# Kernel tuning notes

Hardware: AMD Instinct MI355X
Metric: run time of the kernel (lower is better)

Reference implementation:

```python
import jax, jax.numpy as jnp
import numpy as np

B, N, D, DH = 2, 512, 64, 64


def _lin_params(key, din, dout):
    kw, kb = jax.random.split(key)
    bound = 1.0 / np.sqrt(din)
    W = jax.random.uniform(kw, (din, dout), jnp.float32, -bound, bound)
    b = jax.random.uniform(kb, (dout,), jnp.float32, -bound, bound)
    return W, b


def setup_inputs() -> dict:
    key = jax.random.key(0)
    ks = jax.random.split(key, 11)
    inp = {
        "x": jax.random.normal(ks[0], (B, N, D), jnp.float32),
        "e": jax.random.normal(ks[1], (B, N, N, D), jnp.float32),
    }
    # node-to-node self-attention: Linear(d, d_head)
    inp["Wq1"], inp["bq1"] = _lin_params(ks[2], D, DH)
    inp["Wk1"], inp["bk1"] = _lin_params(ks[3], D, DH)
    inp["Wv1"], inp["bv1"] = _lin_params(ks[4], D, DH)
    # node-to-edge cross-attention
    inp["Wqe"], inp["bqe"] = _lin_params(ks[5], D, DH)   # Q_edge: Linear(d, d_head) on e
    inp["Wkn"], inp["bkn"] = _lin_params(ks[6], DH, DH)  # K_node: Linear(d_head, d_head)
    inp["Wvn"], inp["bvn"] = _lin_params(ks[7], DH, DH)  # V_node
    # edge-to-node cross-attention (all Linear(d_head, d_head))
    inp["Wqn"], inp["bqn"] = _lin_params(ks[8], DH, DH)
    inp["Wke"], inp["bke"] = _lin_params(ks[9], DH, DH)
    inp["Wve"], inp["bve"] = _lin_params(ks[10], DH, DH)
    return inp


def _forward(x, e, Wq1, bq1, Wk1, bk1, Wv1, bv1,
             Wqe, bqe, Wkn, bkn, Wvn, bvn,
             Wqn, bqn, Wke, bke, Wve, bve):
    sqrt_d = jnp.sqrt(jnp.asarray(DH, x.dtype))
    lin = lambda z, W, b: z @ W + b

    # --- self-attention node-to-node: x (B,N,d) -> x_hat (B,N,d_head) ---
    Q = lin(x, Wq1, bq1)
    K = lin(x, Wk1, bk1)
    V = lin(x, Wv1, bv1)
    A = jax.nn.softmax(jnp.einsum('bnd,bmd->bnm', Q, K) / sqrt_d, axis=-1)
    x_hat = jnp.einsum('bnm,bmd->bnd', A, V)

    # --- cross-attention node-to-edge: update e (B,N,N,d) -> e_new (B,N,N,d_head) ---
    Qe = lin(e, Wqe, bqe)                 # (B,N,N,dh)
    Kn = lin(x_hat, Wkn, bkn)             # (B,N,dh)
    Vn = lin(x_hat, Wvn, bvn)
    Si = jnp.einsum('bijd,bjd->bij', Qe, Kn) / sqrt_d  # K_i[b,i,j] = Kn[b,j]
    Sj = jnp.einsum('bijd,bid->bij', Qe, Kn) / sqrt_d  # K_j[b,i,j] = Kn[b,i]
    # Att_i/(Att_i+Att_j) = sigmoid(Si - Sj)
    Ai = jax.nn.sigmoid(Si - Sj)
    Aj = 1.0 - Ai
    e_new = Ai[..., None] * Vn[:, None, :, :] + Aj[..., None] * Vn[:, :, None, :]

    # --- cross-attention edge-to-node: x_new (B,N,d_head) ---
    Qn = lin(x_hat, Wqn, bqn)             # (B,N,dh)
    Ke = lin(e_new, Wke, bke)             # (B,N,N,dh)
    Ve = lin(e_new, Wve, bve)
    S = jnp.einsum('bid,bijd->bij', Qn, Ke) / sqrt_d
    A2 = jax.nn.softmax(S, axis=2)
    x_new = jnp.einsum('bij,bijd->bid', A2, Ve)
    return x_new, e_new


def reference(x, e, Wq1, bq1, Wk1, bk1, Wv1, bv1,
              Wqe, bqe, Wkn, bkn, Wvn, bvn,
              Wqn, bqn, Wke, bke, Wve, bve):
    return _forward(x, e, Wq1, bq1, Wk1, bk1, Wv1, bv1,
                    Wqe, bqe, Wkn, bkn, Wvn, bvn,
                    Wqn, bqn, Wke, bke, Wve, bve)
```

## Files before the change

kernel.cpp:

```cpp
#include <hip/hip_runtime.h>
#include <math.h>

#define NN 512
#define RR 1024

typedef float f4 __attribute__((ext_vector_type(4)));

__global__ __launch_bounds__(256) void prep_kernel(
    const float* __restrict__ x,
    const float* __restrict__ Wq1, const float* __restrict__ bq1,
    const float* __restrict__ Wk1, const float* __restrict__ bk1,
    const float* __restrict__ Wv1, const float* __restrict__ bv1,
    const float* __restrict__ Wkn, const float* __restrict__ bkn,
    const float* __restrict__ Wvn, const float* __restrict__ bvn,
    const float* __restrict__ Wqe, const float* __restrict__ bqe,
    const float* __restrict__ Wke, const float* __restrict__ Wve,
    float* __restrict__ Q, float* __restrict__ K, float* __restrict__ V,
    float* __restrict__ M_P, float* __restrict__ c_P,
    float* __restrict__ M_ke, float* __restrict__ c_ke,
    float* __restrict__ M_ve, float* __restrict__ c_ve,
    float* __restrict__ vq0, float* __restrict__ s0p)
{
    __shared__ float sh[14528];
    const int t = threadIdx.x;

    if (blockIdx.x < 3) {
        const int m = blockIdx.x;
        float* As = sh;
        float* Bs = sh + 4160;
        float* va = sh + 8320;
        float* vb = sh + 8384;
        const float* A  = (m == 0) ? Wkn : Wvn;
        const float* aV = (m == 0) ? bkn : bvn;
        const float* B  = (m == 0) ? Wqe : (m == 1 ? Wke : Wve);
#pragma unroll
        for (int p = 0; p < 16; ++p) {
            const int idx = p * 256 + t;
            const int r = idx >> 6, cc = idx & 63;
            As[r * 65 + cc] = A[idx];
            if (m == 0) Bs[r * 65 + cc] = B[idx];
            else        Bs[cc * 65 + r] = B[idx];
        }
        if (t < 64) { va[t] = aV[t]; vb[t] = bqe[t]; }
        __syncthreads();

        const int b = t & 63, g = t >> 6;
        float acc[16];
#pragma unroll
        for (int aa = 0; aa < 16; ++aa) acc[aa] = 0.f;
        for (int k = 0; k < 64; ++k) {
            const float bv = Bs[b * 65 + k];
#pragma unroll
            for (int aa = 0; aa < 16; ++aa)
                acc[aa] = fmaf(As[(g * 16 + aa) * 65 + k], bv, acc[aa]);
        }
        float* M = (m == 0) ? M_P : (m == 1 ? M_ke : M_ve);
#pragma unroll
        for (int aa = 0; aa < 16; ++aa)
            M[(g * 16 + aa) * 64 + b] = acc[aa];

        if (t < 64) {
            float cb = 0.f;
            for (int k = 0; k < 64; ++k) cb = fmaf(va[k], Bs[t * 65 + k], cb);
            float* C = (m == 0) ? c_P : (m == 1 ? c_ke : c_ve);
            C[t] = cb;
            if (m == 0) {
                float q = 0.f;
                for (int k = 0; k < 64; ++k) q = fmaf(As[t * 65 + k], vb[k], q);
                vq0[t] = q * 0.125f;
            }
        }
        if (m == 0 && t == 0) {
            float s = 0.f;
            for (int k = 0; k < 64; ++k) s += vb[k] * va[k];
            *s0p = s * 0.125f;
        }
    } else {
        const int rb = (blockIdx.x - 3) * 32;
        float* Ws0 = sh;
        float* Ws1 = sh + 4096;
        float* Ws2 = sh + 8192;
        float* xs  = sh + 12288;
        float* bs0 = sh + 14336;
        float* bs1 = sh + 14400;
        float* bs2 = sh + 14464;
#pragma unroll
        for (int p = 0; p < 4; ++p) {
            const int idx = p * 256 + t;
            ((f4*)Ws0)[idx] = ((const f4*)Wq1)[idx];
            ((f4*)Ws1)[idx] = ((const f4*)Wk1)[idx];
            ((f4*)Ws2)[idx] = ((const f4*)Wv1)[idx];
        }
        ((f4*)xs)[t]       = ((const f4*)(x + rb * 64))[t];
        ((f4*)xs)[t + 256] = ((const f4*)(x + rb * 64))[t + 256];
        if (t < 64) { bs0[t] = bq1[t]; bs1[t] = bk1[t]; bs2[t] = bv1[t]; }
        __syncthreads();

        const int d = t & 63, g = t >> 6;
        float a0[8], a1[8], a2[8];
#pragma unroll
        for (int r = 0; r < 8; ++r) { a0[r] = bs0[d]; a1[r] = bs1[d]; a2[r] = bs2[d]; }
        for (int k4 = 0; k4 < 16; ++k4) {
            float w0[4], w1[4], w2[4];
#pragma unroll
            for (int kk = 0; kk < 4; ++kk) {
                w0[kk] = Ws0[(k4 * 4 + kk) * 64 + d];
                w1[kk] = Ws1[(k4 * 4 + kk) * 64 + d];
                w2[kk] = Ws2[(k4 * 4 + kk) * 64 + d];
            }
#pragma unroll
            for (int r = 0; r < 8; ++r) {
                const f4 xv = ((const f4*)xs)[(g * 8 + r) * 16 + k4];
                a0[r] = fmaf(xv.x, w0[0], fmaf(xv.y, w0[1], fmaf(xv.z, w0[2], fmaf(xv.w, w0[3], a0[r]))));
                a1[r] = fmaf(xv.x, w1[0], fmaf(xv.y, w1[1], fmaf(xv.z, w1[2], fmaf(xv.w, w1[3], a1[r]))));
                a2[r] = fmaf(xv.x, w2[0], fmaf(xv.y, w2[1], fmaf(xv.z, w2[2], fmaf(xv.w, w2[3], a2[r]))));
            }
        }
#pragma unroll
        for (int r = 0; r < 8; ++r) {
            Q[(rb + g * 8 + r) * 64 + d] = a0[r];
            K[(rb + g * 8 + r) * 64 + d] = a1[r];
            V[(rb + g * 8 + r) * 64 + d] = a2[r];
        }
    }
}

__global__ __launch_bounds__(256) void selfattn4_kernel(
    const float* __restrict__ Q, const float* __restrict__ K,
    const float* __restrict__ V, float* __restrict__ xhat)
{
    const int rb = blockIdx.x * 4;
    const int b  = rb >> 9;
    const int t  = threadIdx.x;
    const int w  = t >> 6, l = t & 63;

    __shared__ float qs[4 * 64];
    __shared__ float p[4 * 512];

    qs[t] = Q[rb * 64 + t];
    __syncthreads();

#pragma unroll
    for (int half = 0; half < 2; ++half) {
        const int j = half * 256 + t;
        const f4* kr = (const f4*)(K + (size_t)(b * NN + j) * 64);
        float s0 = 0.f, s1 = 0.f, s2 = 0.f, s3 = 0.f;
#pragma unroll
        for (int u = 0; u < 16; ++u) {
            const f4 kv = kr[u];
            const f4 qa = ((const f4*)qs)[u];
            const f4 qb = ((const f4*)(qs + 64))[u];
            const f4 qc = ((const f4*)(qs + 128))[u];
            const f4 qd = ((const f4*)(qs + 192))[u];
            s0 += kv.x * qa.x + kv.y * qa.y + kv.z * qa.z + kv.w * qa.w;
            s1 += kv.x * qb.x + kv.y * qb.y + kv.z * qb.z + kv.w * qb.w;
            s2 += kv.x * qc.x + kv.y * qc.y + kv.z * qc.z + kv.w * qc.w;
            s3 += kv.x * qd.x + kv.y * qd.y + kv.z * qd.z + kv.w * qd.w;
        }
        p[0 * 512 + j] = s0 * 0.125f;
        p[1 * 512 + j] = s1 * 0.125f;
        p[2 * 512 + j] = s2 * 0.125f;
        p[3 * 512 + j] = s3 * 0.125f;
    }
    __syncthreads();

    float* prw = p + w * 512;
    float v[8];
#pragma unroll
    for (int z = 0; z < 8; ++z) v[z] = prw[l + z * 64];
    float mx = v[0];
#pragma unroll
    for (int z = 1; z < 8; ++z) mx = fmaxf(mx, v[z]);
#pragma unroll
    for (int o = 1; o < 64; o <<= 1) mx = fmaxf(mx, __shfl_xor(mx, o));
    float se = 0.f;
#pragma unroll
    for (int z = 0; z < 8; ++z) { v[z] = expf(v[z] - mx); se += v[z]; prw[l + z * 64] = v[z]; }
#pragma unroll
    for (int o = 1; o < 64; o <<= 1) se += __shfl_xor(se, o);
    const float inv = 1.f / se;
    __syncthreads();

    const float* Vb = V + (size_t)b * NN * 64;
    float a0 = 0.f, a1 = 0.f, a2 = 0.f, a3 = 0.f;
    const f4* pw4 = (const f4*)prw;
    for (int j4 = 0; j4 < 128; ++j4) {
        const f4 pv = pw4[j4];
        const int j = j4 * 4;
        a0 = fmaf(pv.x, Vb[(j + 0) * 64 + l], a0);
        a1 = fmaf(pv.y, Vb[(j + 1) * 64 + l], a1);
        a2 = fmaf(pv.z, Vb[(j + 2) * 64 + l], a2);
        a3 = fmaf(pv.w, Vb[(j + 3) * 64 + l], a3);
    }
    xhat[(size_t)(rb + w) * 64 + l] = ((a0 + a1) + (a2 + a3)) * inv;
}

__global__ __launch_bounds__(256) void affine5_kernel(
    const float* __restrict__ xhat,
    const float* __restrict__ Wqn, const float* __restrict__ bqn,
    const float* __restrict__ Wvn, const float* __restrict__ bvn,
    const float* __restrict__ M_P, const float* __restrict__ c_P,
    const float* __restrict__ M_ke, const float* __restrict__ c_ke,
    const float* __restrict__ M_ve, const float* __restrict__ c_ve,
    const float* __restrict__ vq0, const float* __restrict__ s0p,
    float* __restrict__ Qn, float* __restrict__ Vn, float* __restrict__ P,
    float* __restrict__ VnWke, float* __restrict__ VnWve, float* __restrict__ q0)
{
    const int t = threadIdx.x;
    const int rb = blockIdx.x * 32;
    const int m = blockIdx.y;
    const float* W; const float* c; float* o;
    if (m == 0)      { W = Wqn;  c = bqn;  o = Qn; }
    else if (m == 1) { W = Wvn;  c = bvn;  o = Vn; }
    else if (m == 2) { W = M_P;  c = c_P;  o = P; }
    else if (m == 3) { W = M_ke; c = c_ke; o = VnWke; }
    else             { W = M_ve; c = c_ve; o = VnWve; }
    __shared__ float Ws[4096], xs[2048], cs[64], vq0s[64];
#pragma unroll
    for (int p = 0; p < 4; ++p) ((f4*)Ws)[p * 256 + t] = ((const f4*)W)[p * 256 + t];
    ((f4*)xs)[t]       = ((const f4*)(xhat + rb * 64))[t];
    ((f4*)xs)[t + 256] = ((const f4*)(xhat + rb * 64))[t + 256];
    if (t < 64) { cs[t] = c[t]; if (m == 0) vq0s[t] = vq0[t]; }
    __syncthreads();

    const int d = t & 63, g = t >> 6;
    float acc[8];
#pragma unroll
    for (int r = 0; r < 8; ++r) acc[r] = cs[d];
    for (int k4 = 0; k4 < 16; ++k4) {
        float w[4];
#pragma unroll
        for (int kk = 0; kk < 4; ++kk) w[kk] = Ws[(k4 * 4 + kk) * 64 + d];
#pragma unroll
        for (int r = 0; r < 8; ++r) {
            const f4 xv = ((const f4*)xs)[(g * 8 + r) * 16 + k4];
            acc[r] = fmaf(xv.x, w[0], fmaf(xv.y, w[1], fmaf(xv.z, w[2], fmaf(xv.w, w[3], acc[r]))));
        }
    }
#pragma unroll
    for (int r = 0; r < 8; ++r) o[(rb + g * 8 + r) * 64 + d] = acc[r];

    if (m == 0) {
        const int row = t >> 3, seg = t & 7;
        float part = 0.f;
#pragma unroll
        for (int kk = 0; kk < 8; ++kk)
            part = fmaf(xs[row * 64 + seg * 8 + kk], vq0s[seg * 8 + kk], part);
        part += __shfl_xor(part, 1);
        part += __shfl_xor(part, 2);
        part += __shfl_xor(part, 4);
        if (seg == 0) q0[rb + row] = part + s0p[0];
    }
}

__global__ __launch_bounds__(256, 4) void edge_kernel(
    const float* __restrict__ e, const float* __restrict__ P,
    const float* __restrict__ q0, const float* __restrict__ Vn,
    const float* __restrict__ Qn, const float* __restrict__ VnWke,
    const float* __restrict__ VnWve,
    float* __restrict__ e_new,
    float* __restrict__ Epart, float* __restrict__ Gpart, float* __restrict__ Wpart)
{
    const int blk = blockIdx.x;
    const int bi = blk >> 3;
    const int jc = blk & 7;
    const int b  = bi >> 9;
    const int t  = threadIdx.x;
    const int r  = t >> 4;
    const int k  = t & 15;

    const f4* erow  = (const f4*)(e     + (size_t)bi * NN * 64);
    f4*       enrow = (f4*)      (e_new + (size_t)bi * NN * 64);
    const f4* Prow  = (const f4*)P     + (size_t)b * NN * 16;
    const f4* Vrow  = (const f4*)Vn    + (size_t)b * NN * 16;
    const f4* Krow  = (const f4*)VnWke + (size_t)b * NN * 16;
    const f4* Wvrow = (const f4*)VnWve + (size_t)b * NN * 16;
    const float* q0b = q0 + b * NN;

    const int j0 = jc * 64 + r;
    const int j1 = j0 + 16, j2 = j0 + 32, j3 = j0 + 48;

    const f4 ev0 = erow[j0 * 16 + k];
    const f4 ev1 = erow[j1 * 16 + k];
    const f4 ev2 = erow[j2 * 16 + k];
    const f4 ev3 = erow[j3 * 16 + k];

    const float q0i = q0[bi];
    const f4 pi4 = ((const f4*)P)[bi * 16 + k];
    const f4 vi4 = ((const f4*)Vn)[bi * 16 + k];
    const f4 qn4 = ((const f4*)Qn)[bi * 16 + k];
    const f4 wi4 = ((const f4*)VnWke)[bi * 16 + k];
    float uii = qn4.x * wi4.x + qn4.y * wi4.y + qn4.z * wi4.z + qn4.w * wi4.w;
    uii += __shfl_xor(uii, 1);
    uii += __shfl_xor(uii, 2);
    uii += __shfl_xor(uii, 4);
    uii += __shfl_xor(uii, 8);
    uii *= 0.125f;

    float Eacc = 0.f, Gacc = 0.f;
    f4 Wacc = {0.f, 0.f, 0.f, 0.f};

#define EDGE_ITER(EV, J)                                                        \
    {                                                                           \
        const f4 pj = Prow[(J) * 16 + k];                                       \
        const f4 wj = Krow[(J) * 16 + k];                                       \
        const f4 vj = Vrow[(J) * 16 + k];                                       \
        const f4 wv = Wvrow[(J) * 16 + k];                                      \
        const float qj = q0b[(J)];                                              \
        float s = EV.x * (pj.x - pi4.x) + EV.y * (pj.y - pi4.y)                 \
                + EV.z * (pj.z - pi4.z) + EV.w * (pj.w - pi4.w);                \
        float uu = qn4.x * wj.x + qn4.y * wj.y + qn4.z * wj.z + qn4.w * wj.w;   \
        s  += __shfl_xor(s, 1);  uu += __shfl_xor(uu, 1);                       \
        s  += __shfl_xor(s, 2);  uu += __shfl_xor(uu, 2);                       \
        s  += __shfl_xor(s, 4);  uu += __shfl_xor(uu, 4);                       \
        s  += __shfl_xor(s, 8);  uu += __shfl_xor(uu, 8);                       \
        const float ai = 1.f / (1.f + expf(-(s * 0.125f + qj - q0i)));          \
        f4 en;                                                                  \
        en.x = fmaf(ai, vj.x - vi4.x, vi4.x);                                   \
        en.y = fmaf(ai, vj.y - vi4.y, vi4.y);                                   \
        en.z = fmaf(ai, vj.z - vi4.z, vi4.z);                                   \
        en.w = fmaf(ai, vj.w - vi4.w, vi4.w);                                   \
        __builtin_nontemporal_store(en, enrow + (J) * 16 + k);                  \
        const float ex  = expf(ai * (uu * 0.125f - uii));                       \
        const float aex = ai * ex;                                              \
        Eacc += ex;                                                             \
        Gacc += aex;                                                            \
        Wacc.x = fmaf(aex, wv.x, Wacc.x);                                       \
        Wacc.y = fmaf(aex, wv.y, Wacc.y);                                       \
        Wacc.z = fmaf(aex, wv.z, Wacc.z);                                       \
        Wacc.w = fmaf(aex, wv.w, Wacc.w);                                       \
    }

    EDGE_ITER(ev0, j0)
    EDGE_ITER(ev1, j1)
    EDGE_ITER(ev2, j2)
    EDGE_ITER(ev3, j3)
#undef EDGE_ITER

    Eacc += __shfl_xor(Eacc, 16);  Eacc += __shfl_xor(Eacc, 32);
    Gacc += __shfl_xor(Gacc, 16);  Gacc += __shfl_xor(Gacc, 32);
    Wacc.x += __shfl_xor(Wacc.x, 16);  Wacc.x += __shfl_xor(Wacc.x, 32);
    Wacc.y += __shfl_xor(Wacc.y, 16);  Wacc.y += __shfl_xor(Wacc.y, 32);
    Wacc.z += __shfl_xor(Wacc.z, 16);  Wacc.z += __shfl_xor(Wacc.z, 32);
    Wacc.w += __shfl_xor(Wacc.w, 16);  Wacc.w += __shfl_xor(Wacc.w, 32);

    __shared__ float Wred[4][65];
    __shared__ float EG[8];
    const int l = t & 63, w = t >> 6;
    if (l < 16) {
        Wred[w][l * 4 + 0] = Wacc.x;
        Wred[w][l * 4 + 1] = Wacc.y;
        Wred[w][l * 4 + 2] = Wacc.z;
        Wred[w][l * 4 + 3] = Wacc.w;
        if (l == 0) { EG[w] = Eacc; EG[4 + w] = Gacc; }
    }
    __syncthreads();
    if (t < 64) {
        const float Wsum = Wred[0][t] + Wred[1][t] + Wred[2][t] + Wred[3][t];
        Wpart[((size_t)jc * RR + bi) * 64 + t] = Wsum;
        if (t == 0) {
            Epart[jc * RR + bi] = EG[0] + EG[1] + EG[2] + EG[3];
            Gpart[jc * RR + bi] = EG[4] + EG[5] + EG[6] + EG[7];
        }
    }
}

__global__ __launch_bounds__(256) void final4_kernel(
    const float* __restrict__ Epart, const float* __restrict__ Gpart,
    const float* __restrict__ Wpart, const float* __restrict__ VnWve,
    const float* __restrict__ bve, float* __restrict__ x_new)
{
    const int bi = blockIdx.x * 4 + (threadIdx.x >> 6);
    const int t = threadIdx.x & 63;
    float Wsum = 0.f;
#pragma unroll
    for (int jc = 0; jc < 8; ++jc)
        Wsum += Wpart[((size_t)jc * RR + bi) * 64 + t];
    float E = 0.f, G = 0.f;
#pragma unroll
    for (int jc = 0; jc < 8; ++jc) {
        E += Epart[jc * RR + bi];
        G += Gpart[jc * RR + bi];
    }
    const float inv = 1.f / E;
    x_new[(size_t)bi * 64 + t] = bve[t] + VnWve[(size_t)bi * 64 + t] * (1.f - G * inv)
                               + Wsum * inv;
}

extern "C" void kernel_launch(void* const* d_in, const int* in_sizes, int n_in,
                              void* d_out, int out_size, void* d_ws, size_t ws_size,
                              hipStream_t stream) {
    const float* x   = (const float*)d_in[0];
    const float* e   = (const float*)d_in[1];
    const float* Wq1 = (const float*)d_in[2];  const float* bq1 = (const float*)d_in[3];
    const float* Wk1 = (const float*)d_in[4];  const float* bk1 = (const float*)d_in[5];
    const float* Wv1 = (const float*)d_in[6];  const float* bv1 = (const float*)d_in[7];
    const float* Wqe = (const float*)d_in[8];  const float* bqe = (const float*)d_in[9];
    const float* Wkn = (const float*)d_in[10]; const float* bkn = (const float*)d_in[11];
    const float* Wvn = (const float*)d_in[12]; const float* bvn = (const float*)d_in[13];
    const float* Wqn = (const float*)d_in[14]; const float* bqn = (const float*)d_in[15];
    const float* Wke = (const float*)d_in[16];
    const float* Wve = (const float*)d_in[18]; const float* bve = (const float*)d_in[19];

    float* out = (float*)d_out;
    float* x_new = out;
    float* e_new = out + 2 * NN * 64;

    float* ws = (float*)d_ws;
    float* Q     = ws;
    float* K     = Q + RR * 64;
    float* V     = K + RR * 64;
    float* xhat  = V + RR * 64;
    float* Qn    = xhat + RR * 64;
    float* Vn    = Qn + RR * 64;
    float* P     = Vn + RR * 64;
    float* VnWke = P + RR * 64;
    float* VnWve = VnWke + RR * 64;
    float* q0    = VnWve + RR * 64;
    float* M_P   = q0 + RR;
    float* M_ke  = M_P + 4096;
    float* M_ve  = M_ke + 4096;
    float* c_P   = M_ve + 4096;
    float* c_ke  = c_P + 64;
    float* c_ve  = c_ke + 64;
    float* vq0   = c_ve + 64;
    float* s0    = vq0 + 64;
    float* Epart = s0 + 64;
    float* Gpart = Epart + 8 * RR;
    float* Wpart = Gpart + 8 * RR;

    prep_kernel<<<35, 256, 0, stream>>>(x, Wq1, bq1, Wk1, bk1, Wv1, bv1,
                                        Wkn, bkn, Wvn, bvn, Wqe, bqe, Wke, Wve,
                                        Q, K, V,
                                        M_P, c_P, M_ke, c_ke, M_ve, c_ve, vq0, s0);
    selfattn4_kernel<<<RR / 4, 256, 0, stream>>>(Q, K, V, xhat);
    affine5_kernel<<<dim3(32, 5), 256, 0, stream>>>(xhat, Wqn, bqn, Wvn, bvn,
                                                    M_P, c_P, M_ke, c_ke, M_ve, c_ve,
                                                    vq0, s0,
                                                    Qn, Vn, P, VnWke, VnWve, q0);
    edge_kernel<<<RR * 8, 256, 0, stream>>>(e, P, q0, Vn, Qn, VnWke, VnWve,
                                            e_new, Epart, Gpart, Wpart);
    final4_kernel<<<RR / 4, 256, 0, stream>>>(Epart, Gpart, Wpart, VnWve, bve, x_new);
}
```

Before: 82.62 us.

## Process four rows per edge block to reuse per-j loads

Each edge_kernel block now handles four consecutive i rows for one j chunk instead of one, so the per-j loads of P, Vn, VnWke, VnWve and q0 are shared across four rows, and the grid shrinks fourfold. The j loop runs four iterations, each loading four e vectors. This cuts redundant gather traffic and block count but raises register pressure and lowers the number of e loads in flight per thread before compute, which may hurt latency hiding in a bandwidth-bound kernel.

```diff
diff --git a/kernel.cpp b/kernel.cpp
--- a/kernel.cpp
+++ b/kernel.cpp
@@ -262,105 +262,125 @@
     float* __restrict__ Epart, float* __restrict__ Gpart, float* __restrict__ Wpart)
 {
     const int blk = blockIdx.x;
-    const int bi = blk >> 3;
-    const int jc = blk & 7;
-    const int b  = bi >> 9;
-    const int t  = threadIdx.x;
-    const int r  = t >> 4;
-    const int k  = t & 15;
-
-    const f4* erow  = (const f4*)(e     + (size_t)bi * NN * 64);
-    f4*       enrow = (f4*)      (e_new + (size_t)bi * NN * 64);
+    const int bi0 = (blk >> 3) * 4;
+    const int jc  = blk & 7;
+    const int b   = bi0 >> 9;
+    const int t = threadIdx.x;
+    const int r = t >> 4, k = t & 15;
+    const int w = t >> 6, l = t & 63;
+
     const f4* Prow  = (const f4*)P     + (size_t)b * NN * 16;
     const f4* Vrow  = (const f4*)Vn    + (size_t)b * NN * 16;
     const f4* Krow  = (const f4*)VnWke + (size_t)b * NN * 16;
     const f4* Wvrow = (const f4*)VnWve + (size_t)b * NN * 16;
     const float* q0b = q0 + b * NN;
 
-    const int j0 = jc * 64 + r;
-    const int j1 = j0 + 16, j2 = j0 + 32, j3 = j0 + 48;
-
-    const f4 ev0 = erow[j0 * 16 + k];
-    const f4 ev1 = erow[j1 * 16 + k];
-    const f4 ev2 = erow[j2 * 16 + k];
-    const f4 ev3 = erow[j3 * 16 + k];
-
-    const float q0i = q0[bi];
-    const f4 pi4 = ((const f4*)P)[bi * 16 + k];
-    const f4 vi4 = ((const f4*)Vn)[bi * 16 + k];
-    const f4 qn4 = ((const f4*)Qn)[bi * 16 + k];
-    const f4 wi4 = ((const f4*)VnWke)[bi * 16 + k];
-    float uii = qn4.x * wi4.x + qn4.y * wi4.y + qn4.z * wi4.z + qn4.w * wi4.w;
-    uii += __shfl_xor(uii, 1);
-    uii += __shfl_xor(uii, 2);
-    uii += __shfl_xor(uii, 4);
-    uii += __shfl_xor(uii, 8);
-    uii *= 0.125f;
-
-    float Eacc = 0.f, Gacc = 0.f;
-    f4 Wacc = {0.f, 0.f, 0.f, 0.f};
-
-#define EDGE_ITER(EV, J)                                                        \
-    {                                                                           \
-        const f4 pj = Prow[(J) * 16 + k];                                       \
-        const f4 wj = Krow[(J) * 16 + k];                                       \
-        const f4 vj = Vrow[(J) * 16 + k];                                       \
-        const f4 wv = Wvrow[(J) * 16 + k];                                      \
-        const float qj = q0b[(J)];                                              \
-        float s = EV.x * (pj.x - pi4.x) + EV.y * (pj.y - pi4.y)                 \
-                + EV.z * (pj.z - pi4.z) + EV.w * (pj.w - pi4.w);                \
-        float uu = qn4.x * wj.x + qn4.y * wj.y + qn4.z * wj.z + qn4.w * wj.w;   \
-        s  += __shfl_xor(s, 1);  uu += __shfl_xor(uu, 1);                       \
-        s  += __shfl_xor(s, 2);  uu += __shfl_xor(uu, 2);                       \
-        s  += __shfl_xor(s, 4);  uu += __shfl_xor(uu, 4);                       \
-        s  += __shfl_xor(s, 8);  uu += __shfl_xor(uu, 8);                       \
-        const float ai = 1.f / (1.f + expf(-(s * 0.125f + qj - q0i)));          \
-        f4 en;                                                                  \
-        en.x = fmaf(ai, vj.x - vi4.x, vi4.x);                                   \
-        en.y = fmaf(ai, vj.y - vi4.y, vi4.y);                                   \
-        en.z = fmaf(ai, vj.z - vi4.z, vi4.z);                                   \
-        en.w = fmaf(ai, vj.w - vi4.w, vi4.w);                                   \
-        __builtin_nontemporal_store(en, enrow + (J) * 16 + k);                  \
-        const float ex  = expf(ai * (uu * 0.125f - uii));                       \
-        const float aex = ai * ex;                                              \
-        Eacc += ex;                                                             \
-        Gacc += aex;                                                            \
-        Wacc.x = fmaf(aex, wv.x, Wacc.x);                                       \
-        Wacc.y = fmaf(aex, wv.y, Wacc.y);                                       \
-        Wacc.z = fmaf(aex, wv.z, Wacc.z);                                       \
-        Wacc.w = fmaf(aex, wv.w, Wacc.w);                                       \
-    }
-
-    EDGE_ITER(ev0, j0)
-    EDGE_ITER(ev1, j1)
-    EDGE_ITER(ev2, j2)
-    EDGE_ITER(ev3, j3)
-#undef EDGE_ITER
-
-    Eacc += __shfl_xor(Eacc, 16);  Eacc += __shfl_xor(Eacc, 32);
-    Gacc += __shfl_xor(Gacc, 16);  Gacc += __shfl_xor(Gacc, 32);
-    Wacc.x += __shfl_xor(Wacc.x, 16);  Wacc.x += __shfl_xor(Wacc.x, 32);
-    Wacc.y += __shfl_xor(Wacc.y, 16);  Wacc.y += __shfl_xor(Wacc.y, 32);
-    Wacc.z += __shfl_xor(Wacc.z, 16);  Wacc.z += __shfl_xor(Wacc.z, 32);
-    Wacc.w += __shfl_xor(Wacc.w, 16);  Wacc.w += __shfl_xor(Wacc.w, 32);
-
-    __shared__ float Wred[4][65];
-    __shared__ float EG[8];
-    const int l = t & 63, w = t >> 6;
+    f4 pi4[4], vi4[4], qn4[4];
+    float q0i[4], uii[4];
+#pragma unroll
+    for (int ii = 0; ii < 4; ++ii) {
+        const int bi = bi0 + ii;
+        pi4[ii] = ((const f4*)P)[bi * 16 + k];
+        vi4[ii] = ((const f4*)Vn)[bi * 16 + k];
+        qn4[ii] = ((const f4*)Qn)[bi * 16 + k];
+        const f4 wi = ((const f4*)VnWke)[bi * 16 + k];
+        float u = qn4[ii].x * wi.x + qn4[ii].y * wi.y + qn4[ii].z * wi.z + qn4[ii].w * wi.w;
+        u += __shfl_xor(u, 1);
+        u += __shfl_xor(u, 2);
+        u += __shfl_xor(u, 4);
+        u += __shfl_xor(u, 8);
+        uii[ii] = u * 0.125f;
+        q0i[ii] = q0[bi];
+    }
+
+    float Eacc[4] = {0.f, 0.f, 0.f, 0.f};
+    float Gacc[4] = {0.f, 0.f, 0.f, 0.f};
+    f4 Wacc[4];
+#pragma unroll
+    for (int ii = 0; ii < 4; ++ii) Wacc[ii] = (f4){0.f, 0.f, 0.f, 0.f};
+
+    for (int it = 0; it < 4; ++it) {
+        const int j = jc * 64 + it * 16 + r;
+        const f4 pj = Prow[j * 16 + k];
+        const f4 wj = Krow[j * 16 + k];
+        const f4 vj = Vrow[j * 16 + k];
+        const f4 wv = Wvrow[j * 16 + k];
+        const float qj = q0b[j];
+        f4 ev[4];
+#pragma unroll
+        for (int ii = 0; ii < 4; ++ii)
+            ev[ii] = ((const f4*)(e + (size_t)(bi0 + ii) * NN * 64))[j * 16 + k];
+
+        float sv[4], uv[4];
+#pragma unroll
+        for (int ii = 0; ii < 4; ++ii) {
+            sv[ii] = ev[ii].x * (pj.x - pi4[ii].x) + ev[ii].y * (pj.y - pi4[ii].y)
+                   + ev[ii].z * (pj.z - pi4[ii].z) + ev[ii].w * (pj.w - pi4[ii].w);
+            uv[ii] = qn4[ii].x * wj.x + qn4[ii].y * wj.y
+                   + qn4[ii].z * wj.z + qn4[ii].w * wj.w;
+        }
+#pragma unroll
+        for (int o = 1; o <= 8; o <<= 1) {
+#pragma unroll
+            for (int ii = 0; ii < 4; ++ii) {
+                sv[ii] += __shfl_xor(sv[ii], o);
+                uv[ii] += __shfl_xor(uv[ii], o);
+            }
+        }
+#pragma unroll
+        for (int ii = 0; ii < 4; ++ii) {
+            const float ai = 1.f / (1.f + expf(-(sv[ii] * 0.125f + qj - q0i[ii])));
+            f4 en;
+            en.x = fmaf(ai, vj.x - vi4[ii].x, vi4[ii].x);
+            en.y = fmaf(ai, vj.y - vi4[ii].y, vi4[ii].y);
+            en.z = fmaf(ai, vj.z - vi4[ii].z, vi4[ii].z);
+            en.w = fmaf(ai, vj.w - vi4[ii].w, vi4[ii].w);
+            __builtin_nontemporal_store(en,
+                (f4*)(e_new + (size_t)(bi0 + ii) * NN * 64) + j * 16 + k);
+            const float ex  = expf(ai * (uv[ii] * 0.125f - uii[ii]));
+            const float aex = ai * ex;
+            Eacc[ii] += ex;
+            Gacc[ii] += aex;
+            Wacc[ii].x = fmaf(aex, wv.x, Wacc[ii].x);
+            Wacc[ii].y = fmaf(aex, wv.y, Wacc[ii].y);
+            Wacc[ii].z = fmaf(aex, wv.z, Wacc[ii].z);
+            Wacc[ii].w = fmaf(aex, wv.w, Wacc[ii].w);
+        }
+    }
+
+#pragma unroll
+    for (int ii = 0; ii < 4; ++ii) {
+        Eacc[ii] += __shfl_xor(Eacc[ii], 16);  Eacc[ii] += __shfl_xor(Eacc[ii], 32);
+        Gacc[ii] += __shfl_xor(Gacc[ii], 16);  Gacc[ii] += __shfl_xor(Gacc[ii], 32);
+        Wacc[ii].x += __shfl_xor(Wacc[ii].x, 16);  Wacc[ii].x += __shfl_xor(Wacc[ii].x, 32);
+        Wacc[ii].y += __shfl_xor(Wacc[ii].y, 16);  Wacc[ii].y += __shfl_xor(Wacc[ii].y, 32);
+        Wacc[ii].z += __shfl_xor(Wacc[ii].z, 16);  Wacc[ii].z += __shfl_xor(Wacc[ii].z, 32);
+        Wacc[ii].w += __shfl_xor(Wacc[ii].w, 16);  Wacc[ii].w += __shfl_xor(Wacc[ii].w, 32);
+    }
+
+    __shared__ float Wred[4][4][65];
+    __shared__ float EGs[2][4][4];
     if (l < 16) {
-        Wred[w][l * 4 + 0] = Wacc.x;
-        Wred[w][l * 4 + 1] = Wacc.y;
-        Wred[w][l * 4 + 2] = Wacc.z;
-        Wred[w][l * 4 + 3] = Wacc.w;
-        if (l == 0) { EG[w] = Eacc; EG[4 + w] = Gacc; }
+#pragma unroll
+        for (int ii = 0; ii < 4; ++ii) {
+            Wred[ii][w][l * 4 + 0] = Wacc[ii].x;
+            Wred[ii][w][l * 4 + 1] = Wacc[ii].y;
+            Wred[ii][w][l * 4 + 2] = Wacc[ii].z;
+            Wred[ii][w][l * 4 + 3] = Wacc[ii].w;
+            if (l == 0) { EGs[0][ii][w] = Eacc[ii]; EGs[1][ii][w] = Gacc[ii]; }
+        }
     }
     __syncthreads();
-    if (t < 64) {
-        const float Wsum = Wred[0][t] + Wred[1][t] + Wred[2][t] + Wred[3][t];
-        Wpart[((size_t)jc * RR + bi) * 64 + t] = Wsum;
-        if (t == 0) {
-            Epart[jc * RR + bi] = EG[0] + EG[1] + EG[2] + EG[3];
-            Gpart[jc * RR + bi] = EG[4] + EG[5] + EG[6] + EG[7];
+    {
+        const int ii = t >> 6, d = t & 63;
+        const float Wsum = Wred[ii][0][d] + Wred[ii][1][d]
+                         + Wred[ii][2][d] + Wred[ii][3][d];
+        Wpart[((size_t)jc * RR + bi0 + ii) * 64 + d] = Wsum;
+        if (d == 0) {
+            Epart[jc * RR + bi0 + ii] = EGs[0][ii][0] + EGs[0][ii][1]
+                                      + EGs[0][ii][2] + EGs[0][ii][3];
+            Gpart[jc * RR + bi0 + ii] = EGs[1][ii][0] + EGs[1][ii][1]
+                                      + EGs[1][ii][2] + EGs[1][ii][3];
         }
     }
 }
@@ -438,7 +458,7 @@
                                                     M_P, c_P, M_ke, c_ke, M_ve, c_ve,
                                                     vq0, s0,
                                                     Qn, Vn, P, VnWke, VnWve, q0);
-    edge_kernel<<<RR * 8, 256, 0, stream>>>(e, P, q0, Vn, Qn, VnWke, VnWve,
-                                            e_new, Epart, Gpart, Wpart);
+    edge_kernel<<<(RR / 4) * 8, 256, 0, stream>>>(e, P, q0, Vn, Qn, VnWke, VnWve,
+                                                  e_new, Epart, Gpart, Wpart);
     final4_kernel<<<RR / 4, 256, 0, stream>>>(Epart, Gpart, Wpart, VnWve, bve, x_new);
 }
```

Result: slower. 84.77 us (+2.6%).
